# Kernel tuning notes

Measured on AMD Instinct MI355X. Metric: run time of the kernel, lower is better.

The kernel has to match this reference:

```python
import jax, jax.numpy as jnp
import numpy as np

BINS = 256

def _conv_x(t, k):
    # t: [N,1,H,W], k: [3] tap filter along width, 'same' padding
    return jax.lax.conv_general_dilated(t, k.reshape(1, 1, 1, 3), (1, 1), [(0, 0), (1, 1)])

def _conv_y(t, k):
    # t: [N,1,H,W], k: [3] tap filter along height, 'same' padding
    return jax.lax.conv_general_dilated(t, k.reshape(1, 1, 3, 1), (1, 1), [(1, 1), (0, 0)])

def calc_invCR(x):
    # Vectorized equivalent of the per-slice torch.histc loop:
    # 256-bin histogram over [-1,1] per (batch*channel) slice, Shannon entropy in bits / 8.
    n, _, h, w = x.shape
    res = h * w
    xf = x.reshape(n, res)
    valid = ((xf >= -1.0) & (xf <= 1.0)).astype(jnp.float32)
    # bin index; value exactly == max (1.0) falls into the last bin, matching torch.histc
    bins = jnp.clip(jnp.floor((xf + 1.0) * (BINS / 2.0)), 0, BINS - 1).astype(jnp.int32)
    counts = jnp.zeros((n, BINS), jnp.float32).at[jnp.arange(n)[:, None], bins].add(valid)
    p = counts / res
    ent = jnp.sum(jnp.where(p > 0, -p * jnp.log2(jnp.where(p > 0, p, 1.0)), 0.0))
    return ent / (8.0 * n)

def _forward(x, px, ux, cx, rx, py, uy, cy, ry):
    b, c, h, w = x.shape
    img = x.reshape(b * c, 1, h, w)
    cur = img
    xos, yos = [], []
    for lvl in range(5):
        xe, xo = cur[:, :, :, ::2], cur[:, :, :, 1::2]
        xo = xo - _conv_x(xe, px)
        xe = xe + _conv_x(xo, ux)
        xo = xo - _conv_x(xe, cx)
        xe = xe + _conv_x(xo, rx)
        ye, yo = xe[:, :, ::2, :], xe[:, :, 1::2, :]
        yo = yo - _conv_y(ye, py)
        if lvl < 2:
            ye = ye + _conv_y(yo, uy)
        # levels 3-5 in the source apply update_y to the (discarded) x?e tensor
        # (`x3e = x3e + self.update_y(x3o)`); that result is never used, so it is a
        # no-op for the output and is faithfully omitted here.
        yo = yo - _conv_y(ye, cy)
        ye = ye + _conv_y(yo, ry)
        xos.append(xo)
        yos.append(yo)
        cur = ye
    out = cur
    for xo, yo in zip(reversed(xos), reversed(yos)):
        out = jnp.concatenate((jnp.concatenate((out, yo), axis=2), xo), axis=3)
    deltas = jnp.fmod(out + 1.0, 2.0) - 1.0  # wrap residuals into [-1,1]
    loss1 = 255.0 * jnp.sqrt(jnp.mean(jnp.square(deltas)))
    loss0 = 255.0 * jnp.sqrt(jnp.mean(jnp.square(img)))
    invCR0 = calc_invCR(img)
    invCR1 = calc_invCR(deltas)
    return loss1, loss0, invCR0, invCR1

def setup_inputs() -> dict:
    key = jax.random.key(0)
    ks = jax.random.split(key, 9)
    inp = {"x": jax.random.uniform(ks[0], (32, 3, 512, 512), jnp.float32)}
    for i, name in enumerate(["px", "ux", "cx", "rx", "py", "uy", "cy", "ry"]):
        inp[name] = 0.25 * jax.random.normal(ks[i + 1], (3,), jnp.float32)
    return inp

def reference(x, px, ux, cx, rx, py, uy, cy, ry):
    return _forward(x, px, ux, cx, rx, py, uy, cy, ry)
```

## Files before the change

### kernel.cpp

```cpp
#include <hip/hip_runtime.h>
#include <math.h>

#define NIMG 96
#define NSLOT 1024
#define RES_INV (1.0f / 262144.0f)

__device__ __forceinline__ float wrap1(float v) {
  float t = v + 1.0f;
  return t - 2.0f * truncf(t * 0.5f) - 1.0f;
}
__device__ __forceinline__ int bin_of(float v) {
  float b = floorf((v + 1.0f) * 128.0f);
  b = fminf(fmaxf(b, 0.0f), 255.0f);
  return (int)b;
}

template<int P, int SEGP, int USE_UY, int DO_IMG>
__global__ void __launch_bounds__(256) klift_fused(
    const float* __restrict__ src, float* __restrict__ ye_out,
    const float* __restrict__ kpx, const float* __restrict__ kux,
    const float* __restrict__ kcx, const float* __restrict__ krx,
    const float* __restrict__ kpy, const float* __restrict__ kuy,
    const float* __restrict__ kcy, const float* __restrict__ kry,
    double* __restrict__ partial,
    unsigned* __restrict__ hist_img, unsigned* __restrict__ hist_delta)
{
  constexpr int W2 = 64 * P;
  constexpr int H2 = W2;
  constexpr int H  = 2 * H2;
  constexpr int NP = SEGP + 8;
  constexpr int NR = 2 * NP;
  __shared__ float tile[NR][W2];
  __shared__ unsigned shd[256];
  __shared__ unsigned shi[256];

  const int t = threadIdx.x, w = t >> 6, lane = t & 63;
  const int img = blockIdx.y;
  const int R0 = blockIdx.x * SEGP;
  const int Rend = (R0 + SEGP < H2) ? R0 + SEGP : H2;
  const int base_in = 2 * R0 - 8;

  shd[t] = 0;
  if (DO_IMG) shi[t] = 0;
  __syncthreads();

  const float px0 = kpx[0], px1 = kpx[1], px2 = kpx[2];
  const float ux0 = kux[0], ux1 = kux[1], ux2 = kux[2];
  const float cx0 = kcx[0], cx1 = kcx[1], cx2 = kcx[2];
  const float rx0 = krx[0], rx1 = krx[1], rx2 = krx[2];
  const float py0 = kpy[0], py1 = kpy[1], py2 = kpy[2];
  const float uy0 = kuy[0], uy1 = kuy[1], uy2 = kuy[2];
  const float cy0 = kcy[0], cy1 = kcy[1], cy2 = kcy[2];
  const float ry0 = kry[0], ry1 = kry[1], ry2 = kry[2];

  const float* ip = src + (size_t)img * H * (2 * W2);
  float sqi = 0.f, sqd = 0.f;

  auto stepm = [&](float (&d)[P], float (&s)[P], float k0, float k1, float k2, float sgn) {
    float L = __shfl_up(s[P - 1], 1); if (lane == 0) L = 0.f;
    float R = __shfl_down(s[0], 1);   if (lane == 63) R = 0.f;
    float prev = L;
#pragma unroll
    for (int j = 0; j < P; j++) {
      float nxt = (j == P - 1) ? R : s[(j + 1) < P ? (j + 1) : 0];
      d[j] += sgn * (k0 * prev + k1 * s[j] + k2 * nxt);
      prev = s[j];
    }
  };
  auto ldrow = [&](int lr, float4& A, float4& B) {
    const int gin = base_in + lr;
    if (gin >= 0 && gin < H) {
      const float* rp = ip + (size_t)gin * (2 * W2) + lane * (2 * P);
      A = *(const float4*)rp;
      if (P == 4) B = *(const float4*)(rp + 4);
    } else {
      A = make_float4(0.f, 0.f, 0.f, 0.f);
      B = make_float4(0.f, 0.f, 0.f, 0.f);
    }
  };

  const int wcol = (P == 4) ? ((lane ^ ((lane >> 3) & 7)) * 4) : (lane * 2);

  float4 cA, cB, nA, nB;
  ldrow(w, cA, cB);
  for (int lr = w; lr < NR; lr += 4) {
    if (lr + 4 < NR) ldrow(lr + 4, nA, nB);
    const int gin = base_in + lr;
    const bool owned = (gin >= 2 * R0) && (gin < 2 * Rend);
    float e[P], o[P];
    e[0] = cA.x; o[0] = cA.y;
    if (P >= 2) { e[P > 1 ? 1 : 0] = cA.z; o[P > 1 ? 1 : 0] = cA.w; }
    if (P == 4) {
      e[P > 2 ? 2 : 0] = cB.x; o[P > 2 ? 2 : 0] = cB.y;
      e[P > 3 ? 3 : 0] = cB.z; o[P > 3 ? 3 : 0] = cB.w;
    }
    if (DO_IMG && owned) {
#pragma unroll
      for (int j = 0; j < P; j++) {
        sqi += e[j] * e[j] + o[j] * o[j];
        atomicAdd(&shi[bin_of(e[j])], 1u);
        atomicAdd(&shi[bin_of(o[j])], 1u);
      }
    }
    stepm(o, e, px0, px1, px2, -1.f);
    stepm(e, o, ux0, ux1, ux2,  1.f);
    stepm(o, e, cx0, cx1, cx2, -1.f);
    stepm(e, o, rx0, rx1, rx2,  1.f);
    if (P == 4) {
      *(float4*)&tile[lr][wcol] =
          make_float4(e[0], e[P > 1 ? 1 : 0], e[P > 2 ? 2 : 0], e[P > 3 ? 3 : 0]);
    } else {
      *(float2*)&tile[lr][wcol] = make_float2(e[0], e[P > 1 ? 1 : 0]);
    }
    if (owned) {
#pragma unroll
      for (int j = 0; j < P; j++) {
        float d = wrap1(o[j]);
        sqd += d * d;
        if (d >= -1.f && d <= 1.f) atomicAdd(&shd[bin_of(d)], 1u);
      }
    }
    cA = nA; cB = nB;
  }
  __syncthreads();

  {
    constexpr int NSP = 256 / W2;
    constexpr int LEN = SEGP / NSP;
    constexpr int WIN = LEN + 8;
    const int col = t % W2;
    const int half = t / W2;
    const int q0 = half * LEN;
    int colr;
    if (P == 4) {
      const int ch = (col >> 2) ^ ((col >> 5) & 7);
      colr = (ch << 2) | (col & 3);
    } else colr = col;

    float ee[WIN], oo[WIN];
#pragma unroll
    for (int q = 0; q < WIN; ++q) {
      ee[q] = tile[2 * (q0 + q)][colr];
      oo[q] = tile[2 * (q0 + q) + 1][colr];
    }
#pragma unroll
    for (int q = 0; q < WIN; ++q) {
      float U = (q > 0) ? ee[q - 1] : 0.f;
      float D = (q < WIN - 1) ? ee[q + 1] : 0.f;
      oo[q] -= py0 * U + py1 * ee[q] + py2 * D;
    }
    if (USE_UY) {
#pragma unroll
      for (int q = 0; q < WIN; ++q) {
        float U = (q > 0) ? oo[q - 1] : 0.f;
        float D = (q < WIN - 1) ? oo[q + 1] : 0.f;
        ee[q] += uy0 * U + uy1 * oo[q] + uy2 * D;
      }
    }
#pragma unroll
    for (int q = 0; q < WIN; ++q) {
      float U = (q > 0) ? ee[q - 1] : 0.f;
      float D = (q < WIN - 1) ? ee[q + 1] : 0.f;
      oo[q] -= cy0 * U + cy1 * ee[q] + cy2 * D;
    }
#pragma unroll
    for (int q = 0; q < WIN; ++q) {
      float U = (q > 0) ? oo[q - 1] : 0.f;
      float D = (q < WIN - 1) ? oo[q + 1] : 0.f;
      ee[q] += ry0 * U + ry1 * oo[q] + ry2 * D;
    }
    float* outp = ye_out + (size_t)img * H2 * W2 + col;
#pragma unroll
    for (int q = 4; q < 4 + LEN; ++q) {
      const int g = R0 + q0 + q - 4;
      float d = wrap1(oo[q]);
      sqd += d * d;
      if (d >= -1.f && d <= 1.f) atomicAdd(&shd[bin_of(d)], 1u);
      outp[(size_t)g * W2] = ee[q];
    }
  }

  for (int off = 32; off; off >>= 1) {
    sqd += __shfl_down(sqd, off);
    if (DO_IMG) sqi += __shfl_down(sqi, off);
  }
  if (lane == 0) {
    const int bid = blockIdx.x + blockIdx.y * gridDim.x;
    const int slot = (bid * 4 + w) & (NSLOT - 1);
    atomicAdd(&partial[NSLOT + slot], (double)sqd);
    if (DO_IMG) atomicAdd(&partial[slot], (double)sqi);
  }
  __syncthreads();
  unsigned hd = shd[t];
  if (hd) atomicAdd(&hist_delta[img * 256 + t], hd);
  if (DO_IMG) {
    unsigned hi = shi[t];
    if (hi) atomicAdd(&hist_img[img * 256 + t], hi);
  }
}

__global__ void __launch_bounds__(256) klift_tail(
    const float* __restrict__ src,
    const float* __restrict__ kpx, const float* __restrict__ kux,
    const float* __restrict__ kcx, const float* __restrict__ krx,
    const float* __restrict__ kpy, const float* __restrict__ kcy,
    const float* __restrict__ kry,
    double* __restrict__ partial, unsigned* __restrict__ hist_delta)
{
  __shared__ float tile[128][129];
  __shared__ unsigned shd[256];
  const int t = threadIdx.x;
  const int img = blockIdx.x;
  shd[t] = 0;

  const float* sp = src + (size_t)img * 128 * 128;
  for (int idx = t; idx < 128 * 32; idx += 256) {
    const int r = idx >> 5, c4 = (idx & 31) << 2;
    float4 v = *(const float4*)(sp + r * 128 + c4);
    tile[r][c4] = v.x; tile[r][c4 + 1] = v.y;
    tile[r][c4 + 2] = v.z; tile[r][c4 + 3] = v.w;
  }
  const float px0 = kpx[0], px1 = kpx[1], px2 = kpx[2];
  const float ux0 = kux[0], ux1 = kux[1], ux2 = kux[2];
  const float cx0 = kcx[0], cx1 = kcx[1], cx2 = kcx[2];
  const float rx0 = krx[0], rx1 = krx[1], rx2 = krx[2];
  const float pc0 = kpy[0] + kcy[0], pc1 = kpy[1] + kcy[1], pc2 = kpy[2] + kcy[2];
  const float ry0 = kry[0], ry1 = kry[1], ry2 = kry[2];
  float sqd = 0.f;
  __syncthreads();

  for (int l = 0; l < 3; ++l) {
    const int s = 1 << l, n = 128 >> l, half = n >> 1;
    const int totx = n * half;

    for (int idx = t; idx < totx; idx += 256) {
      const int r = (idx / half) * s, c = idx % half;
      float L = (c > 0) ? tile[r][(2 * c - 2) * s] : 0.f;
      float M = tile[r][2 * c * s];
      float R = (c < half - 1) ? tile[r][(2 * c + 2) * s] : 0.f;
      tile[r][(2 * c + 1) * s] -= px0 * L + px1 * M + px2 * R;
    }
    __syncthreads();
    for (int idx = t; idx < totx; idx += 256) {
      const int r = (idx / half) * s, c = idx % half;
      float L = (c > 0) ? tile[r][(2 * c - 1) * s] : 0.f;
      float M = tile[r][(2 * c + 1) * s];
      float R = (c < half - 1) ? tile[r][(2 * c + 3) * s] : 0.f;
      tile[r][2 * c * s] += ux0 * L + ux1 * M + ux2 * R;
    }
    __syncthreads();
    for (int idx = t; idx < totx; idx += 256) {
      const int r = (idx / half) * s, c = idx % half;
      float L = (c > 0) ? tile[r][(2 * c - 2) * s] : 0.f;
      float M = tile[r][2 * c * s];
      float R = (c < half - 1) ? tile[r][(2 * c + 2) * s] : 0.f;
      tile[r][(2 * c + 1) * s] -= cx0 * L + cx1 * M + cx2 * R;
    }
    __syncthreads();
    for (int idx = t; idx < totx; idx += 256) {
      const int r = (idx / half) * s, c = idx % half;
      float L = (c > 0) ? tile[r][(2 * c - 1) * s] : 0.f;
      float M = tile[r][(2 * c + 1) * s];
      float R = (c < half - 1) ? tile[r][(2 * c + 3) * s] : 0.f;
      tile[r][2 * c * s] += rx0 * L + rx1 * M + rx2 * R;
    }
    __syncthreads();
    for (int idx = t; idx < totx; idx += 256) {
      const int r = (idx / half) * s, c = idx % half;
      float d = wrap1(tile[r][(2 * c + 1) * s]);
      sqd += d * d;
      if (d >= -1.f && d <= 1.f) atomicAdd(&shd[bin_of(d)], 1u);
    }
    const int toty = half * half;
    for (int idx = t; idx < toty; idx += 256) {
      const int r = idx / half, j = idx % half, col = j * 2 * s;
      float U = (r > 0) ? tile[(2 * r - 2) * s][col] : 0.f;
      float M = tile[(2 * r) * s][col];
      float D = (r < half - 1) ? tile[(2 * r + 2) * s][col] : 0.f;
      tile[(2 * r + 1) * s][col] -= pc0 * U + pc1 * M + pc2 * D;
    }
    __syncthreads();
    for (int idx = t; idx < toty; idx += 256) {
      const int r = idx / half, j = idx % half, col = j * 2 * s;
      float U = (r > 0) ? tile[(2 * r - 1) * s][col] : 0.f;
      float M = tile[(2 * r + 1) * s][col];
      float D = (r < half - 1) ? tile[(2 * r + 3) * s][col] : 0.f;
      tile[(2 * r) * s][col] += ry0 * U + ry1 * M + ry2 * D;
    }
    __syncthreads();
    for (int idx = t; idx < toty; idx += 256) {
      const int r = idx / half, j = idx % half, col = j * 2 * s;
      float d = wrap1(tile[(2 * r + 1) * s][col]);
      sqd += d * d;
      if (d >= -1.f && d <= 1.f) atomicAdd(&shd[bin_of(d)], 1u);
      if (l == 2) {
        float d2 = wrap1(tile[(2 * r) * s][col]);
        sqd += d2 * d2;
        if (d2 >= -1.f && d2 <= 1.f) atomicAdd(&shd[bin_of(d2)], 1u);
      }
    }
    __syncthreads();
  }

  for (int off = 32; off; off >>= 1) sqd += __shfl_down(sqd, off);
  __shared__ float swv[4];
  if ((t & 63) == 0) swv[t >> 6] = sqd;
  __syncthreads();
  if (t == 0) {
    double tot = (double)swv[0] + swv[1] + swv[2] + swv[3];
    atomicAdd(&partial[NSLOT + (img & (NSLOT - 1))], tot);
  }
  unsigned hd = shd[t];
  if (hd) atomicAdd(&hist_delta[img * 256 + t], hd);
}

__global__ void __launch_bounds__(256) kfinal(
    const double* __restrict__ partial,
    const unsigned* __restrict__ hist_img,
    const unsigned* __restrict__ hist_delta,
    float* __restrict__ out)
{
  __shared__ double sI[256], sD[256], sPi[256], sPd[256];
  const int t = threadIdx.x;
  double entI = 0.0, entD = 0.0;
  for (int img = 0; img < NIMG; ++img) {
    unsigned ci = hist_img[img * 256 + t];
    if (ci) { float p = (float)ci * RES_INV; entI += (double)(-p * log2f(p)); }
    unsigned cd = hist_delta[img * 256 + t];
    if (cd) { float p = (float)cd * RES_INV; entD += (double)(-p * log2f(p)); }
  }
  double pi = 0.0, pd = 0.0;
  for (int s = t; s < NSLOT; s += 256) {
    pi += partial[s];
    pd += partial[NSLOT + s];
  }
  sI[t] = entI; sD[t] = entD; sPi[t] = pi; sPd[t] = pd;
  __syncthreads();
  for (int s = 128; s; s >>= 1) {
    if (t < s) {
      sI[t] += sI[t + s]; sD[t] += sD[t + s];
      sPi[t] += sPi[t + s]; sPd[t] += sPd[t + s];
    }
    __syncthreads();
  }
  if (t == 0) {
    const double tot = (double)NIMG * 262144.0;
    out[0] = (float)(255.0 * sqrt(sPd[0] / tot));
    out[1] = (float)(255.0 * sqrt(sPi[0] / tot));
    out[2] = (float)(sI[0] / (8.0 * NIMG));
    out[3] = (float)(sD[0] / (8.0 * NIMG));
  }
}

extern "C" void kernel_launch(void* const* d_in, const int* in_sizes, int n_in,
                              void* d_out, int out_size, void* d_ws, size_t ws_size,
                              hipStream_t stream)
{
  const float* x  = (const float*)d_in[0];
  const float* px = (const float*)d_in[1];
  const float* ux = (const float*)d_in[2];
  const float* cx = (const float*)d_in[3];
  const float* rx = (const float*)d_in[4];
  const float* py = (const float*)d_in[5];
  const float* uy = (const float*)d_in[6];
  const float* cy = (const float*)d_in[7];
  const float* ry = (const float*)d_in[8];
  float* out = (float*)d_out;

  char* ws = (char*)d_ws;
  double*   partial    = (double*)ws;
  unsigned* hist_img   = (unsigned*)(ws + 2 * NSLOT * 8);
  unsigned* hist_delta = (unsigned*)(ws + 2 * NSLOT * 8 + NIMG * 256 * 4);
  float* buf0 = (float*)(ws + (1 << 18));
  float* buf1 = (float*)(ws + (1 << 18) + ((size_t)32 << 20));

  hipMemsetAsync(ws, 0, 2 * NSLOT * 8 + 2 * NIMG * 256 * 4, stream);

  klift_fused<4, 16, 1, 1><<<dim3(16, NIMG), 256, 0, stream>>>(
      x, buf0, px, ux, cx, rx, py, uy, cy, ry, partial, hist_img, hist_delta);
  klift_fused<2, 16, 1, 0><<<dim3(8, NIMG), 256, 0, stream>>>(
      buf0, buf1, px, ux, cx, rx, py, uy, cy, ry, partial, hist_img, hist_delta);
  klift_tail<<<NIMG, 256, 0, stream>>>(buf1, px, ux, cx, rx, py, cy, ry,
                                       partial, hist_delta);
  kfinal<<<1, 256, 0, stream>>>(partial, hist_img, hist_delta, out);
}
```

Baseline: 109.2 us.

## Move level three into fused lifting kernel and shrink tail to 64x64

Level three of the wavelet lifting now runs through the fused row/column kernel (a P=1 variant with no uy update) instead of the single-block-per-image tail kernel, so the tail only handles a 64x64 tile over two levels. The level-two kernel uses smaller row segments with twice as many blocks, and the row loop is fully unrolled with compile-time ownership and bounds checks. Histogram binning becomes one fma plus truncation and drops the range test, relying on wrapped residuals always lying in [-1,1]. This adds one kernel launch and an extra intermediate buffer, and the bin_fast change assumes inputs are never below -1.

```diff
diff --git a/kernel.cpp b/kernel.cpp
--- a/kernel.cpp
+++ b/kernel.cpp
@@ -9,10 +9,9 @@
   float t = v + 1.0f;
   return t - 2.0f * truncf(t * 0.5f) - 1.0f;
 }
-__device__ __forceinline__ int bin_of(float v) {
-  float b = floorf((v + 1.0f) * 128.0f);
-  b = fminf(fmaxf(b, 0.0f), 255.0f);
-  return (int)b;
+__device__ __forceinline__ int bin_fast(float v) {
+  int b = (int)fmaf(v, 128.0f, 128.0f);
+  return (b > 255) ? 255 : b;
 }
 
 template<int P, int SEGP, int USE_UY, int DO_IMG>
@@ -30,6 +29,7 @@
   constexpr int H  = 2 * H2;
   constexpr int NP = SEGP + 8;
   constexpr int NR = 2 * NP;
+  constexpr int NITER = NR / 4;
   __shared__ float tile[NR][W2];
   __shared__ unsigned shd[256];
   __shared__ unsigned shi[256];
@@ -37,7 +37,6 @@
   const int t = threadIdx.x, w = t >> 6, lane = t & 63;
   const int img = blockIdx.y;
   const int R0 = blockIdx.x * SEGP;
-  const int Rend = (R0 + SEGP < H2) ? R0 + SEGP : H2;
   const int base_in = 2 * R0 - 8;
 
   shd[t] = 0;
@@ -67,26 +66,32 @@
       prev = s[j];
     }
   };
-  auto ldrow = [&](int lr, float4& A, float4& B) {
+  auto ldrow = [&](int lr, float4& A, float4& B, bool chk) {
     const int gin = base_in + lr;
-    if (gin >= 0 && gin < H) {
+    if (!chk || ((unsigned)gin < (unsigned)H)) {
       const float* rp = ip + (size_t)gin * (2 * W2) + lane * (2 * P);
-      A = *(const float4*)rp;
-      if (P == 4) B = *(const float4*)(rp + 4);
+      if (P == 1) { float2 v = *(const float2*)rp; A.x = v.x; A.y = v.y; }
+      else {
+        A = *(const float4*)rp;
+        if (P == 4) B = *(const float4*)(rp + 4);
+      }
     } else {
       A = make_float4(0.f, 0.f, 0.f, 0.f);
       B = make_float4(0.f, 0.f, 0.f, 0.f);
     }
   };
 
-  const int wcol = (P == 4) ? ((lane ^ ((lane >> 3) & 7)) * 4) : (lane * 2);
-
-  float4 cA, cB, nA, nB;
-  ldrow(w, cA, cB);
-  for (int lr = w; lr < NR; lr += 4) {
-    if (lr + 4 < NR) ldrow(lr + 4, nA, nB);
-    const int gin = base_in + lr;
-    const bool owned = (gin >= 2 * R0) && (gin < 2 * Rend);
+  const int wcol = (P == 4) ? ((lane ^ ((lane >> 3) & 7)) * 4)
+                 : (P == 2) ? (lane * 2) : lane;
+
+  float4 cA = make_float4(0.f,0.f,0.f,0.f), cB = cA, nA = cA, nB = cA;
+  ldrow(w, cA, cB, true);
+#pragma unroll
+  for (int i = 0; i < NITER; ++i) {
+    const int lr = w + 4 * i;
+    if (i + 1 < NITER)
+      ldrow(lr + 4, nA, nB, (i + 1 < 2) || (i + 1 >= NITER - 2));
+    const bool owned = (i >= 2) && (i < NITER - 2);
     float e[P], o[P];
     e[0] = cA.x; o[0] = cA.y;
     if (P >= 2) { e[P > 1 ? 1 : 0] = cA.z; o[P > 1 ? 1 : 0] = cA.w; }
@@ -98,8 +103,8 @@
 #pragma unroll
       for (int j = 0; j < P; j++) {
         sqi += e[j] * e[j] + o[j] * o[j];
-        atomicAdd(&shi[bin_of(e[j])], 1u);
-        atomicAdd(&shi[bin_of(o[j])], 1u);
+        atomicAdd(&shi[bin_fast(e[j])], 1u);
+        atomicAdd(&shi[bin_fast(o[j])], 1u);
       }
     }
     stepm(o, e, px0, px1, px2, -1.f);
@@ -109,15 +114,17 @@
     if (P == 4) {
       *(float4*)&tile[lr][wcol] =
           make_float4(e[0], e[P > 1 ? 1 : 0], e[P > 2 ? 2 : 0], e[P > 3 ? 3 : 0]);
+    } else if (P == 2) {
+      *(float2*)&tile[lr][wcol] = make_float2(e[0], e[P > 1 ? 1 : 0]);
     } else {
-      *(float2*)&tile[lr][wcol] = make_float2(e[0], e[P > 1 ? 1 : 0]);
+      tile[lr][wcol] = e[0];
     }
     if (owned) {
 #pragma unroll
       for (int j = 0; j < P; j++) {
         float d = wrap1(o[j]);
         sqd += d * d;
-        if (d >= -1.f && d <= 1.f) atomicAdd(&shd[bin_of(d)], 1u);
+        atomicAdd(&shd[bin_fast(d)], 1u);
       }
     }
     cA = nA; cB = nB;
@@ -175,7 +182,7 @@
       const int g = R0 + q0 + q - 4;
       float d = wrap1(oo[q]);
       sqd += d * d;
-      if (d >= -1.f && d <= 1.f) atomicAdd(&shd[bin_of(d)], 1u);
+      atomicAdd(&shd[bin_fast(d)], 1u);
       outp[(size_t)g * W2] = ee[q];
     }
   }
@@ -199,7 +206,7 @@
   }
 }
 
-__global__ void __launch_bounds__(256) klift_tail(
+__global__ void __launch_bounds__(256) klift_tail64(
     const float* __restrict__ src,
     const float* __restrict__ kpx, const float* __restrict__ kux,
     const float* __restrict__ kcx, const float* __restrict__ krx,
@@ -207,16 +214,16 @@
     const float* __restrict__ kry,
     double* __restrict__ partial, unsigned* __restrict__ hist_delta)
 {
-  __shared__ float tile[128][129];
+  __shared__ float tile[64][65];
   __shared__ unsigned shd[256];
   const int t = threadIdx.x;
   const int img = blockIdx.x;
   shd[t] = 0;
 
-  const float* sp = src + (size_t)img * 128 * 128;
-  for (int idx = t; idx < 128 * 32; idx += 256) {
-    const int r = idx >> 5, c4 = (idx & 31) << 2;
-    float4 v = *(const float4*)(sp + r * 128 + c4);
+  const float* sp = src + (size_t)img * 64 * 64;
+  for (int idx = t; idx < 64 * 16; idx += 256) {
+    const int r = idx >> 4, c4 = (idx & 15) << 2;
+    float4 v = *(const float4*)(sp + r * 64 + c4);
     tile[r][c4] = v.x; tile[r][c4 + 1] = v.y;
     tile[r][c4 + 2] = v.z; tile[r][c4 + 3] = v.w;
   }
@@ -229,8 +236,8 @@
   float sqd = 0.f;
   __syncthreads();
 
-  for (int l = 0; l < 3; ++l) {
-    const int s = 1 << l, n = 128 >> l, half = n >> 1;
+  for (int l = 0; l < 2; ++l) {
+    const int s = 1 << l, n = 64 >> l, half = n >> 1;
     const int totx = n * half;
 
     for (int idx = t; idx < totx; idx += 256) {
@@ -269,7 +276,7 @@
       const int r = (idx / half) * s, c = idx % half;
       float d = wrap1(tile[r][(2 * c + 1) * s]);
       sqd += d * d;
-      if (d >= -1.f && d <= 1.f) atomicAdd(&shd[bin_of(d)], 1u);
+      atomicAdd(&shd[bin_fast(d)], 1u);
     }
     const int toty = half * half;
     for (int idx = t; idx < toty; idx += 256) {
@@ -292,11 +299,11 @@
       const int r = idx / half, j = idx % half, col = j * 2 * s;
       float d = wrap1(tile[(2 * r + 1) * s][col]);
       sqd += d * d;
-      if (d >= -1.f && d <= 1.f) atomicAdd(&shd[bin_of(d)], 1u);
-      if (l == 2) {
+      atomicAdd(&shd[bin_fast(d)], 1u);
+      if (l == 1) {
         float d2 = wrap1(tile[(2 * r) * s][col]);
         sqd += d2 * d2;
-        if (d2 >= -1.f && d2 <= 1.f) atomicAdd(&shd[bin_of(d2)], 1u);
+        atomicAdd(&shd[bin_fast(d2)], 1u);
       }
     }
     __syncthreads();
@@ -371,16 +378,19 @@
   double*   partial    = (double*)ws;
   unsigned* hist_img   = (unsigned*)(ws + 2 * NSLOT * 8);
   unsigned* hist_delta = (unsigned*)(ws + 2 * NSLOT * 8 + NIMG * 256 * 4);
-  float* buf0 = (float*)(ws + (1 << 18));
-  float* buf1 = (float*)(ws + (1 << 18) + ((size_t)32 << 20));
+  float* buf0 = (float*)(ws + (1 << 20));
+  float* buf1 = (float*)(ws + (1 << 20) + ((size_t)32 << 20));
+  float* buf2 = (float*)(ws + (1 << 20) + ((size_t)40 << 20));
 
   hipMemsetAsync(ws, 0, 2 * NSLOT * 8 + 2 * NIMG * 256 * 4, stream);
 
   klift_fused<4, 16, 1, 1><<<dim3(16, NIMG), 256, 0, stream>>>(
       x, buf0, px, ux, cx, rx, py, uy, cy, ry, partial, hist_img, hist_delta);
-  klift_fused<2, 16, 1, 0><<<dim3(8, NIMG), 256, 0, stream>>>(
+  klift_fused<2, 8, 1, 0><<<dim3(16, NIMG), 256, 0, stream>>>(
       buf0, buf1, px, ux, cx, rx, py, uy, cy, ry, partial, hist_img, hist_delta);
-  klift_tail<<<NIMG, 256, 0, stream>>>(buf1, px, ux, cx, rx, py, cy, ry,
-                                       partial, hist_delta);
+  klift_fused<1, 8, 0, 0><<<dim3(8, NIMG), 256, 0, stream>>>(
+      buf1, buf2, px, ux, cx, rx, py, uy, cy, ry, partial, hist_img, hist_delta);
+  klift_tail64<<<NIMG, 256, 0, stream>>>(buf2, px, ux, cx, rx, py, cy, ry,
+                                         partial, hist_delta);
   kfinal<<<1, 256, 0, stream>>>(partial, hist_img, hist_delta, out);
 }
```

Measured after the change: 89.26 us. 1.22x faster.
